# Kernel tuning notes

Measured on AMD Instinct MI355X. Metric: run time of the kernel, lower is better.

Reference implementation:

```python
import jax, jax.numpy as jnp
import numpy as np
from jax import lax

T = 1_000_000  # time steps
K = 64         # hidden states


def setup_inputs() -> dict:
    key = jax.random.key(0)
    k1, k2, k3, k4 = jax.random.split(key, 4)
    return {
        "y": jax.random.normal(k1, (T,), dtype=jnp.float32),
        "transition_logits": jax.random.normal(k2, (K, K), dtype=jnp.float32),
        "mu": jax.random.normal(k3, (K,), dtype=jnp.float32),
        "log_sigma": jax.random.normal(k4, (K,), dtype=jnp.float32) * 0.1,
    }


def _stationary_distribution(P):
    # Solve pi^T P = pi^T with sum(pi) = 1 via a linear system (differentiable).
    k = P.shape[0]
    A = jnp.transpose(P) - jnp.eye(k, dtype=P.dtype)
    A = A.at[-1, :].set(jnp.ones((k,), dtype=P.dtype))
    b = jnp.zeros((k,), dtype=P.dtype).at[-1].set(1.0)
    return jnp.linalg.solve(A, b)


def reference(y, transition_logits, mu, log_sigma):
    # Row-stochastic transition matrix [K, K]
    P = jax.nn.softmax(transition_logits, axis=-1)
    sigma = jnp.exp(log_sigma)  # [K]
    # Univariate Gaussian emission densities g[t, k] = N(y_t; mu_k, sigma_k^2)
    z = (y[:, None] - mu[None, :]) / sigma[None, :]           # [T, K]
    inv_norm = 1.0 / (sigma * jnp.sqrt(2.0 * jnp.pi))         # [K]
    g = jnp.exp(-0.5 * z * z) * inv_norm[None, :]             # [T, K]

    ut0 = _stationary_distribution(P)        # initial (predicted) distribution
    g0 = g[0]
    ft0 = jnp.sum(ut0 * g0)                  # normalizer at t=0
    utt0 = ut0 * g0 / ft0                    # filtered distribution at t=0

    def step(utt, gt):
        ut = utt @ P                         # predict: [K]
        num = ut * gt
        ft = jnp.sum(num)
        utt_new = num / ft                   # update (normalize)
        return utt_new, (ut, ft, utt_new)

    _, (Ut, ft_rest, Utt) = lax.scan(step, utt0, g[1:])

    ut = jnp.concatenate([ut0[None, :], Ut], axis=0)        # [T, K] predicted
    u_norm = jnp.concatenate([utt0[None, :], Utt], axis=0)  # [T, K] filtered
    ft = jnp.concatenate([ft0[None], ft_rest], axis=0)      # [T] normalizers
    return ut, u_norm, ft
```

## Files before the change

kernel.cpp:

```cpp
#include <hip/hip_runtime.h>

#define K 64
#define S_CHUNK 128
#define W_BURN 160
#define BATCH 16

typedef __attribute__((ext_vector_type(4))) _Float16 half4;
typedef __attribute__((ext_vector_type(4))) float f32x4;

__device__ __forceinline__ float waveReduceSum(float v) {
#pragma unroll
    for (int off = 32; off > 0; off >>= 1) v += __shfl_xor(v, off, 64);
    return v;
}

#define WS_P     0
#define WS_PI    4096
#define WS_UTT0  4160
#define WS_ISG   4224
#define WS_NNU   4288
#define WS_L2N   4352

__global__ __launch_bounds__(64) void hmm_setup(
    const float* __restrict__ y, const float* __restrict__ logits,
    const float* __restrict__ mu, const float* __restrict__ log_sigma,
    float* __restrict__ out, float* __restrict__ ws, int T)
{
    __shared__ float P[K][K];
    __shared__ float pib[K];
    const int k = threadIdx.x;

    float row[K]; float m = -3.4e38f;
#pragma unroll
    for (int i = 0; i < K; ++i) { row[i] = logits[k*K + i]; m = fmaxf(m, row[i]); }
    float s = 0.f;
#pragma unroll
    for (int i = 0; i < K; ++i) { row[i] = __expf(row[i] - m); s += row[i]; }
    float inv = 1.0f / s;
#pragma unroll
    for (int i = 0; i < K; ++i) { float p = row[i]*inv; P[k][i] = p; ws[WS_P + k*K + i] = p; }
    __syncthreads();

    pib[k] = 1.0f/64.0f;
    __syncthreads();
    for (int it = 0; it < 64; ++it) {
        float acc = 0.f;
#pragma unroll
        for (int j = 0; j < K; ++j) acc += pib[j]*P[j][k];
        float tot = waveReduceSum(acc);
        acc /= tot;
        __syncthreads();
        pib[k] = acc;
        __syncthreads();
    }
    float pi_k = pib[k];

    float mu_k = mu[k];
    float isg = __expf(-log_sigma[k]);
    float inorm = isg * 0.39894228040143267f;

    ws[WS_PI  + k] = pi_k;
    ws[WS_ISG + k] = isg;
    ws[WS_NNU + k] = -mu_k * isg;
    ws[WS_L2N + k] = __log2f(inorm);

    float y0 = y[0];
    float z = (y0 - mu_k) * isg;
    float g0 = __expf(-0.5f*z*z) * inorm;
    float num = pi_k * g0;
    float ft0 = waveReduceSum(num);
    float utt0 = num / ft0;
    ws[WS_UTT0 + k] = utt0;

    out[k] = pi_k;
    out[(size_t)T*K + k] = utt0;
    if (k == 0) out[(size_t)2*T*K] = ft0;
}

__global__ __launch_bounds__(64) void hmm_scan(
    const float* __restrict__ y, const float* __restrict__ ws,
    float* __restrict__ out, int T)
{
    const int lane = threadIdx.x;
    const int c = lane & 15;
    const int q = lane >> 4;
    const int NCH = (T + S_CHUNK - 1) / S_CHUNK;
    const int cg = blockIdx.x * BATCH + c;
    const int t0 = cg * S_CHUNK;

    half4 a[4][4];
#pragma unroll
    for (int nb = 0; nb < 4; ++nb)
#pragma unroll
        for (int kb = 0; kb < 4; ++kb)
#pragma unroll
            for (int j = 0; j < 4; ++j)
                a[nb][kb][j] = (_Float16)ws[WS_P + (16*kb + 4*q + j)*K + 16*nb + c];

    f32x4 isg_[4], nnu_[4], l2n_[4];
#pragma unroll
    for (int nb = 0; nb < 4; ++nb)
#pragma unroll
        for (int r = 0; r < 4; ++r) {
            int s = 16*nb + 4*q + r;
            isg_[nb][r] = ws[WS_ISG + s];
            nnu_[nb][r] = ws[WS_NNU + s];
            l2n_[nb][r] = ws[WS_L2N + s];
        }

    half4 bfr[4], u0h[4];
#pragma unroll
    for (int kb = 0; kb < 4; ++kb)
#pragma unroll
        for (int j = 0; j < 4; ++j) {
            int s = 16*kb + 4*q + j;
            bfr[kb][j] = (_Float16)ws[WS_PI + s];
            u0h[kb][j] = (_Float16)ws[WS_UTT0 + s];
        }

    const int tlo = (cg == 0) ? 1 : ((cg < NCH) ? 0 : 0x7fffffff);
    int tcur = t0 - W_BURN;

    float* po = out + (size_t)t0 * K + 4*q;
    float* pu = po + (size_t)T * K;
    float* pf = out + (size_t)2 * T * K + t0;

    int ib = min(max(tcur, 0), T - 4);
    f32x4 yv = *(const f32x4*)(y + ib);

#define STEP(OUTP, YCUR) do {                                                  \
    f32x4 acc[4] = {{0.f,0.f,0.f,0.f},{0.f,0.f,0.f,0.f},                       \
                    {0.f,0.f,0.f,0.f},{0.f,0.f,0.f,0.f}};                      \
    _Pragma("unroll")                                                          \
    for (int kb = 0; kb < 4; ++kb) {                                           \
        _Pragma("unroll")                                                      \
        for (int nb = 0; nb < 4; ++nb)                                         \
            acc[nb] = __builtin_amdgcn_mfma_f32_16x16x16f16(                   \
                a[nb][kb], bfr[kb], acc[nb], 0, 0, 0);                         \
    }                                                                          \
    const bool pred = (tcur >= tlo) & (tcur < T);                              \
    if (OUTP && pred) {                                                        \
        _Pragma("unroll")                                                      \
        for (int nb = 0; nb < 4; ++nb)                                         \
            *(f32x4*)(po + 16*nb) = acc[nb];                                   \
    }                                                                          \
    f32x4 nrm[4]; float st = 0.f;                                              \
    _Pragma("unroll")                                                          \
    for (int nb = 0; nb < 4; ++nb) {                                           \
        _Pragma("unroll")                                                      \
        for (int r = 0; r < 4; ++r) {                                          \
            float z  = fmaf(YCUR, isg_[nb][r], nnu_[nb][r]);                   \
            float ag = fmaf(z*z, -0.72134752f, l2n_[nb][r]);                   \
            float g  = __builtin_amdgcn_exp2f(ag);                             \
            nrm[nb][r] = acc[nb][r] * g;                                       \
            st += nrm[nb][r];                                                  \
        }                                                                      \
    }                                                                          \
    st += __shfl_xor(st, 16, 64);                                              \
    st += __shfl_xor(st, 32, 64);                                              \
    const float rs = __builtin_amdgcn_rcpf(st);                                \
    _Pragma("unroll")                                                          \
    for (int nb = 0; nb < 4; ++nb) nrm[nb] *= rs;                              \
    if (OUTP && pred) {                                                        \
        _Pragma("unroll")                                                      \
        for (int nb = 0; nb < 4; ++nb)                                         \
            *(f32x4*)(pu + 16*nb) = nrm[nb];                                   \
        if (lane < 16) *pf = st;                                               \
    }                                                                          \
    _Pragma("unroll")                                                          \
    for (int kb = 0; kb < 4; ++kb) {                                           \
        auto lo = __builtin_amdgcn_cvt_pkrtz(nrm[kb][0], nrm[kb][1]);          \
        auto hi = __builtin_amdgcn_cvt_pkrtz(nrm[kb][2], nrm[kb][3]);          \
        bfr[kb][0] = (_Float16)lo[0]; bfr[kb][1] = (_Float16)lo[1];            \
        bfr[kb][2] = (_Float16)hi[0]; bfr[kb][3] = (_Float16)hi[1];            \
    }                                                                          \
    if (OUTP) { po += K; pu += K; pf += 1; }                                   \
    ++tcur;                                                                    \
} while (0)

#pragma unroll 1
    for (int gi = 0; gi < W_BURN/4; ++gi) {
        int ibn = min(max(tcur + 4, 0), T - 4);
        f32x4 yn = *(const f32x4*)(y + ibn);
        STEP(0, yv[0]); STEP(0, yv[1]); STEP(0, yv[2]); STEP(0, yv[3]);
        yv = yn;
    }
    {
        int ibn = min(max(tcur + 4, 0), T - 4);
        f32x4 yn = *(const f32x4*)(y + ibn);
        STEP(1, yv[0]);
        if (cg == 0) { bfr[0]=u0h[0]; bfr[1]=u0h[1]; bfr[2]=u0h[2]; bfr[3]=u0h[3]; }
        STEP(1, yv[1]); STEP(1, yv[2]); STEP(1, yv[3]);
        yv = yn;
    }
#pragma unroll 1
    for (int gi = 1; gi < S_CHUNK/4; ++gi) {
        int ibn = min(max(tcur + 4, 0), T - 4);
        f32x4 yn = *(const f32x4*)(y + ibn);
        STEP(1, yv[0]); STEP(1, yv[1]); STEP(1, yv[2]); STEP(1, yv[3]);
        yv = yn;
    }
#undef STEP
}

extern "C" void kernel_launch(void* const* d_in, const int* in_sizes, int n_in,
                              void* d_out, int out_size, void* d_ws, size_t ws_size,
                              hipStream_t stream) {
    const float* y      = (const float*)d_in[0];
    const float* logits = (const float*)d_in[1];
    const float* mu     = (const float*)d_in[2];
    const float* lsig   = (const float*)d_in[3];
    float* out = (float*)d_out;
    float* ws  = (float*)d_ws;
    const int T = in_sizes[0];

    hmm_setup<<<1, 64, 0, stream>>>(y, logits, mu, lsig, out, ws, T);

    const int nch  = (T + S_CHUNK - 1) / S_CHUNK;
    const int nblk = (nch + BATCH - 1) / BATCH;
    hmm_scan<<<nblk, 64, 0, stream>>>(y, ws, out, T);
}
```

Before: 229.6 us.

## Defer normalization off the recurrence critical path with power-of-two rescaling

The step no longer normalizes the filtered vector before feeding it to the next matvec. The unnormalized product is fed straight back, and its scale is held in check by folding an exact power-of-two exponent into the emission exponent. The cross-lane sum, reciprocal and the outputs for the previous step are computed while the next step's MFMAs run. The MFMA chain is also split into two independent accumulators to shorten the dependency chain. This moves the shuffle-reduce and rcp latency off the serial chain. In exchange it adds extra bookkeeping, an epilogue store, and the risk of fp16 range or precision problems in the unnormalized values.

```diff
diff --git a/kernel.cpp b/kernel.cpp
--- a/kernel.cpp
+++ b/kernel.cpp
@@ -85,6 +85,7 @@
     const int c = lane & 15;
     const int q = lane >> 4;
     const int NCH = (T + S_CHUNK - 1) / S_CHUNK;
+    (void)NCH;
     const int cg = blockIdx.x * BATCH + c;
     const int t0 = cg * S_CHUNK;
 
@@ -118,63 +119,99 @@
             u0h[kb][j] = (_Float16)ws[WS_UTT0 + s];
         }
 
-    const int tlo = (cg == 0) ? 1 : ((cg < NCH) ? 0 : 0x7fffffff);
+    const int tlo = (cg == 0) ? 1 : 0;
     int tcur = t0 - W_BURN;
 
     float* po = out + (size_t)t0 * K + 4*q;
     float* pu = po + (size_t)T * K;
     float* pf = out + (size_t)2 * T * K + t0;
 
+    float h = 0.25f;
+    float rmP = 1.0f;
+    f32x4 nbP[4] = {{0.f,0.f,0.f,0.f},{0.f,0.f,0.f,0.f},
+                    {0.f,0.f,0.f,0.f},{0.f,0.f,0.f,0.f}};
+
     int ib = min(max(tcur, 0), T - 4);
     f32x4 yv = *(const f32x4*)(y + ib);
 
-#define STEP(OUTP, YCUR) do {                                                  \
-    f32x4 acc[4] = {{0.f,0.f,0.f,0.f},{0.f,0.f,0.f,0.f},                       \
-                    {0.f,0.f,0.f,0.f},{0.f,0.f,0.f,0.f}};                      \
-    _Pragma("unroll")                                                          \
-    for (int kb = 0; kb < 4; ++kb) {                                           \
+#define STEP(OUTC, OUTPV, YCUR) do {                                           \
+                                  \
+    f32x4 accA_[4] = {{0.f,0.f,0.f,0.f},{0.f,0.f,0.f,0.f},                     \
+                      {0.f,0.f,0.f,0.f},{0.f,0.f,0.f,0.f}};                    \
+    f32x4 accB_[4] = {{0.f,0.f,0.f,0.f},{0.f,0.f,0.f,0.f},                     \
+                      {0.f,0.f,0.f,0.f},{0.f,0.f,0.f,0.f}};                    \
+    _Pragma("unroll")                                                          \
+    for (int nb_ = 0; nb_ < 4; ++nb_)                                          \
+        accA_[nb_] = __builtin_amdgcn_mfma_f32_16x16x16f16(a[nb_][0], bfr[0], accA_[nb_], 0,0,0); \
+    _Pragma("unroll")                                                          \
+    for (int nb_ = 0; nb_ < 4; ++nb_)                                          \
+        accB_[nb_] = __builtin_amdgcn_mfma_f32_16x16x16f16(a[nb_][2], bfr[2], accB_[nb_], 0,0,0); \
+    _Pragma("unroll")                                                          \
+    for (int nb_ = 0; nb_ < 4; ++nb_)                                          \
+        accA_[nb_] = __builtin_amdgcn_mfma_f32_16x16x16f16(a[nb_][1], bfr[1], accA_[nb_], 0,0,0); \
+    _Pragma("unroll")                                                          \
+    for (int nb_ = 0; nb_ < 4; ++nb_)                                          \
+        accB_[nb_] = __builtin_amdgcn_mfma_f32_16x16x16f16(a[nb_][3], bfr[3], accB_[nb_], 0,0,0); \
+                         \
+    float s1_ = h + __shfl_xor(h, 16, 64);                                     \
+    float stP_ = s1_ + __shfl_xor(s1_, 32, 64);                                \
+    float rsP_ = __builtin_amdgcn_rcpf(stP_);                                  \
+    float ftprev_ = stP_ * rmP;                                                \
+    unsigned ub_ = __float_as_uint(stP_);                                      \
+    float xf_ = (float)(127 - (int)((ub_ >> 23) & 255u));                      \
+    float mant_ = __uint_as_float((ub_ & 0x007fffffu) | 0x3f800000u);          \
+    float rmN_ = __builtin_amdgcn_rcpf(mant_);                                 \
+                \
+    f32x4 g_[4];                                                               \
+    _Pragma("unroll")                                                          \
+    for (int nb_ = 0; nb_ < 4; ++nb_) {                                        \
+        f32x4 z_ = YCUR * isg_[nb_] + nnu_[nb_];                               \
+        f32x4 ag_ = z_*z_*(-0.72134752f) + l2n_[nb_] + xf_;                    \
         _Pragma("unroll")                                                      \
-        for (int nb = 0; nb < 4; ++nb)                                         \
-            acc[nb] = __builtin_amdgcn_mfma_f32_16x16x16f16(                   \
-                a[nb][kb], bfr[kb], acc[nb], 0, 0, 0);                         \
-    }                                                                          \
-    const bool pred = (tcur >= tlo) & (tcur < T);                              \
-    if (OUTP && pred) {                                                        \
-        _Pragma("unroll")                                                      \
-        for (int nb = 0; nb < 4; ++nb)                                         \
-            *(f32x4*)(po + 16*nb) = acc[nb];                                   \
-    }                                                                          \
-    f32x4 nrm[4]; float st = 0.f;                                              \
-    _Pragma("unroll")                                                          \
-    for (int nb = 0; nb < 4; ++nb) {                                           \
-        _Pragma("unroll")                                                      \
-        for (int r = 0; r < 4; ++r) {                                          \
-            float z  = fmaf(YCUR, isg_[nb][r], nnu_[nb][r]);                   \
-            float ag = fmaf(z*z, -0.72134752f, l2n_[nb][r]);                   \
-            float g  = __builtin_amdgcn_exp2f(ag);                             \
-            nrm[nb][r] = acc[nb][r] * g;                                       \
-            st += nrm[nb][r];                                                  \
+        for (int r_ = 0; r_ < 4; ++r_) g_[nb_][r_] = __builtin_amdgcn_exp2f(ag_[r_]); \
+    }                                                                          \
+                                  \
+    if (OUTPV) {                                                               \
+        const bool pp_ = ((tcur-1) >= tlo) & ((tcur-1) < T);                   \
+        if (pp_) {                                                             \
+            _Pragma("unroll")                                                  \
+            for (int nb_ = 0; nb_ < 4; ++nb_)                                  \
+                *(f32x4*)(pu - K + 16*nb_) = nbP[nb_] * rsP_;                  \
+            if (lane < 16) pf[-1] = ftprev_;                                   \
         }                                                                      \
     }                                                                          \
-    st += __shfl_xor(st, 16, 64);                                              \
-    st += __shfl_xor(st, 32, 64);                                              \
-    const float rs = __builtin_amdgcn_rcpf(st);                                \
-    _Pragma("unroll")                                                          \
-    for (int nb = 0; nb < 4; ++nb) nrm[nb] *= rs;                              \
-    if (OUTP && pred) {                                                        \
-        _Pragma("unroll")                                                      \
-        for (int nb = 0; nb < 4; ++nb)                                         \
-            *(f32x4*)(pu + 16*nb) = nrm[nb];                                   \
-        if (lane < 16) *pf = st;                                               \
-    }                                                                          \
-    _Pragma("unroll")                                                          \
-    for (int kb = 0; kb < 4; ++kb) {                                           \
-        auto lo = __builtin_amdgcn_cvt_pkrtz(nrm[kb][0], nrm[kb][1]);          \
-        auto hi = __builtin_amdgcn_cvt_pkrtz(nrm[kb][2], nrm[kb][3]);          \
-        bfr[kb][0] = (_Float16)lo[0]; bfr[kb][1] = (_Float16)lo[1];            \
-        bfr[kb][2] = (_Float16)hi[0]; bfr[kb][3] = (_Float16)hi[1];            \
-    }                                                                          \
-    if (OUTP) { po += K; pu += K; pf += 1; }                                   \
+                                               \
+    f32x4 acc_[4], nbv_[4];                                                    \
+    _Pragma("unroll")                                                          \
+    for (int nb_ = 0; nb_ < 4; ++nb_) acc_[nb_] = accA_[nb_] + accB_[nb_];     \
+    _Pragma("unroll")                                                          \
+    for (int nb_ = 0; nb_ < 4; ++nb_) nbv_[nb_] = acc_[nb_] * g_[nb_];         \
+    _Pragma("unroll")                                                          \
+    for (int kb_ = 0; kb_ < 4; ++kb_) {                                        \
+        auto lo_ = __builtin_amdgcn_cvt_pkrtz(nbv_[kb_][0], nbv_[kb_][1]);     \
+        auto hi_ = __builtin_amdgcn_cvt_pkrtz(nbv_[kb_][2], nbv_[kb_][3]);     \
+        bfr[kb_][0] = (_Float16)lo_[0]; bfr[kb_][1] = (_Float16)lo_[1];        \
+        bfr[kb_][2] = (_Float16)hi_[0]; bfr[kb_][3] = (_Float16)hi_[1];        \
+    }                                                                          \
+                                          \
+    if (OUTC) {                                                                \
+        const bool pc_ = (tcur >= tlo) & (tcur < T);                           \
+        if (pc_) {                                                             \
+            _Pragma("unroll")                                                  \
+            for (int nb_ = 0; nb_ < 4; ++nb_)                                  \
+                *(f32x4*)(po + 16*nb_) = acc_[nb_] * rsP_;                     \
+        }                                                                      \
+    }                                                                          \
+               \
+    {                                                                          \
+        f32x4 sA_ = nbv_[0] + nbv_[1];                                         \
+        f32x4 sB_ = nbv_[2] + nbv_[3];                                         \
+        f32x4 sC_ = sA_ + sB_;                                                 \
+        h = (sC_[0] + sC_[1]) + (sC_[2] + sC_[3]);                             \
+    }                                                                          \
+    nbP[0]=nbv_[0]; nbP[1]=nbv_[1]; nbP[2]=nbv_[2]; nbP[3]=nbv_[3];            \
+    rmP = rmN_;                                                                \
+    if (OUTC) { po += K; pu += K; pf += 1; }                                   \
     ++tcur;                                                                    \
 } while (0)
 
@@ -182,25 +219,42 @@
     for (int gi = 0; gi < W_BURN/4; ++gi) {
         int ibn = min(max(tcur + 4, 0), T - 4);
         f32x4 yn = *(const f32x4*)(y + ibn);
-        STEP(0, yv[0]); STEP(0, yv[1]); STEP(0, yv[2]); STEP(0, yv[3]);
+        STEP(0,0, yv[0]); STEP(0,0, yv[1]); STEP(0,0, yv[2]); STEP(0,0, yv[3]);
         yv = yn;
     }
     {
         int ibn = min(max(tcur + 4, 0), T - 4);
         f32x4 yn = *(const f32x4*)(y + ibn);
-        STEP(1, yv[0]);
-        if (cg == 0) { bfr[0]=u0h[0]; bfr[1]=u0h[1]; bfr[2]=u0h[2]; bfr[3]=u0h[3]; }
-        STEP(1, yv[1]); STEP(1, yv[2]); STEP(1, yv[3]);
+        STEP(1,0, yv[0]);
+        if (cg == 0) {
+            bfr[0]=u0h[0]; bfr[1]=u0h[1]; bfr[2]=u0h[2]; bfr[3]=u0h[3];
+            h = 0.25f;
+        }
+        STEP(1,1, yv[1]); STEP(1,1, yv[2]); STEP(1,1, yv[3]);
         yv = yn;
     }
 #pragma unroll 1
     for (int gi = 1; gi < S_CHUNK/4; ++gi) {
         int ibn = min(max(tcur + 4, 0), T - 4);
         f32x4 yn = *(const f32x4*)(y + ibn);
-        STEP(1, yv[0]); STEP(1, yv[1]); STEP(1, yv[2]); STEP(1, yv[3]);
+        STEP(1,1, yv[0]); STEP(1,1, yv[1]); STEP(1,1, yv[2]); STEP(1,1, yv[3]);
         yv = yn;
     }
 #undef STEP
+
+    {
+        float s1 = h + __shfl_xor(h, 16, 64);
+        float stL = s1 + __shfl_xor(s1, 32, 64);
+        float rsL = __builtin_amdgcn_rcpf(stL);
+        float ftL = stL * rmP;
+        const bool pp = ((tcur-1) >= tlo) & ((tcur-1) < T);
+        if (pp) {
+#pragma unroll
+            for (int nb = 0; nb < 4; ++nb)
+                *(f32x4*)(pu - K + 16*nb) = nbP[nb] * rsL;
+            if (lane < 16) pf[-1] = ftL;
+        }
+    }
 }
 
 extern "C" void kernel_launch(void* const* d_in, const int* in_sizes, int n_in,
```

Result: no change. 231.2 us (+0.7%).

## Replace MFMA batched scan with per-wave fdot2 matvec via LDS broadcast

Applied to the files above, without the earlier changes.

Restructures the chunked HMM filter so each half-wave owns one chunk and each lane computes two states using packed fp16 dot products against register-resident P columns. The state vector is shared through LDS instead of being fed to MFMA. Normalization is deferred: each step folds an exponent-based rescale into the emission term and emits the previous step's filtered output using the next step's sum. Burn-in drops from 160 to 128 steps and blocks grow to 256 threads, trading MFMA throughput for far more independent chunks in flight and less per-step reduction latency. The extra fp16 sums and deferred scaling add some precision risk.

```diff
diff --git a/kernel.cpp b/kernel.cpp
--- a/kernel.cpp
+++ b/kernel.cpp
@@ -2,16 +2,35 @@
 
 #define K 64
 #define S_CHUNK 128
-#define W_BURN 160
-#define BATCH 16
-
-typedef __attribute__((ext_vector_type(4))) _Float16 half4;
+#define W_BURN 128
+
+typedef __attribute__((ext_vector_type(2))) _Float16 half2v;
+typedef __attribute__((ext_vector_type(8))) _Float16 half8;
 typedef __attribute__((ext_vector_type(4))) float f32x4;
+typedef __attribute__((ext_vector_type(2))) float f32x2;
+typedef __attribute__((ext_vector_type(4))) unsigned u32x4;
+
+#define ONEPK 0x3C003C00u
 
 __device__ __forceinline__ float waveReduceSum(float v) {
 #pragma unroll
     for (int off = 32; off > 0; off >>= 1) v += __shfl_xor(v, off, 64);
     return v;
+}
+
+__device__ __forceinline__ unsigned pkh(float a, float b) {
+    auto t = __builtin_amdgcn_cvt_pkrtz(a, b);
+    return __builtin_bit_cast(unsigned, t);
+}
+
+__device__ __forceinline__ float fdot2(unsigned a, unsigned b, float c) {
+#if __has_builtin(__builtin_amdgcn_fdot2)
+    return __builtin_amdgcn_fdot2(__builtin_bit_cast(half2v, a),
+                                  __builtin_bit_cast(half2v, b), c, false);
+#else
+    half2v x = __builtin_bit_cast(half2v, a), y = __builtin_bit_cast(half2v, b);
+    return c + (float)x[0] * (float)y[0] + (float)x[1] * (float)y[1];
+#endif
 }
 
 #define WS_P     0
@@ -20,6 +39,7 @@
 #define WS_ISG   4224
 #define WS_NNU   4288
 #define WS_L2N   4352
+#define WS_PKP   4480
 
 __global__ __launch_bounds__(64) void hmm_setup(
     const float* __restrict__ y, const float* __restrict__ logits,
@@ -55,6 +75,11 @@
     }
     float pi_k = pib[k];
 
+    unsigned* wsu = (unsigned*)ws;
+#pragma unroll
+    for (int j2 = 0; j2 < 32; ++j2)
+        wsu[WS_PKP + k*32 + j2] = pkh(P[2*j2][k], P[2*j2+1][k]);
+
     float mu_k = mu[k];
     float isg = __expf(-log_sigma[k]);
     float inorm = isg * 0.39894228040143267f;
@@ -77,130 +102,137 @@
     if (k == 0) out[(size_t)2*T*K] = ft0;
 }
 
-__global__ __launch_bounds__(64) void hmm_scan(
+__global__ __launch_bounds__(256, 2) void hmm_scan(
     const float* __restrict__ y, const float* __restrict__ ws,
     float* __restrict__ out, int T)
 {
-    const int lane = threadIdx.x;
-    const int c = lane & 15;
-    const int q = lane >> 4;
-    const int NCH = (T + S_CHUNK - 1) / S_CHUNK;
-    const int cg = blockIdx.x * BATCH + c;
-    const int t0 = cg * S_CHUNK;
-
-    half4 a[4][4];
-#pragma unroll
-    for (int nb = 0; nb < 4; ++nb)
-#pragma unroll
-        for (int kb = 0; kb < 4; ++kb)
-#pragma unroll
-            for (int j = 0; j < 4; ++j)
-                a[nb][kb][j] = (_Float16)ws[WS_P + (16*kb + 4*q + j)*K + 16*nb + c];
-
-    f32x4 isg_[4], nnu_[4], l2n_[4];
-#pragma unroll
-    for (int nb = 0; nb < 4; ++nb)
-#pragma unroll
-        for (int r = 0; r < 4; ++r) {
-            int s = 16*nb + 4*q + r;
-            isg_[nb][r] = ws[WS_ISG + s];
-            nnu_[nb][r] = ws[WS_NNU + s];
-            l2n_[nb][r] = ws[WS_L2N + s];
+    __shared__ __align__(16) unsigned ubuf[4][2][32];
+    const int tid  = threadIdx.x;
+    const int wid  = tid >> 6;
+    const int lane = tid & 63;
+    const int h    = lane >> 5;
+    const int r    = lane & 31;
+    const int s0   = 2 * r;
+    const int wv   = blockIdx.x * 4 + wid;
+    const int cg   = 2 * wv + h;
+    const int t0   = cg * S_CHUNK;
+
+    const unsigned* wsu = (const unsigned*)ws;
+
+    u32x4 P0r[8], P1r[8];
+    {
+        const u32x4* p0 = (const u32x4*)(wsu + WS_PKP + s0 * 32);
+        const u32x4* p1 = (const u32x4*)(wsu + WS_PKP + (s0 + 1) * 32);
+#pragma unroll
+        for (int i = 0; i < 8; ++i) { P0r[i] = p0[i]; P1r[i] = p1[i]; }
+    }
+
+    const float isg0 = ws[WS_ISG + s0], isg1 = ws[WS_ISG + s0 + 1];
+    const float nnu0 = ws[WS_NNU + s0], nnu1 = ws[WS_NNU + s0 + 1];
+    const float l2n0 = ws[WS_L2N + s0], l2n1 = ws[WS_L2N + s0 + 1];
+
+    unsigned* ub = &ubuf[wid][h][0];
+    const u32x4* ubv = (const u32x4*)ub;
+
+    unsigned myu = pkh(ws[WS_PI + s0], ws[WS_PI + s0 + 1]);
+    ub[r] = myu;
+    unsigned u0pk = pkh(ws[WS_UTT0 + s0], ws[WS_UTT0 + s0 + 1]);
+
+    const int tlo = (cg == 0) ? 1 : t0;
+    const bool is_cg0 = (cg == 0);
+    const int t_end = t0 + S_CHUNK;
+
+    float* po = out + (size_t)(t0 - W_BURN) * K + s0;
+    float* pu = po + (size_t)T * K;
+    float* pf = out + (size_t)2 * T * K + (t0 - W_BURN);
+
+    float rcpPrev = 1.0f, sclPrev = 1.0f;
+
+#pragma unroll 1
+    for (int t = t0 - W_BURN; t < t_end; ++t) {
+        int iy = min(max(t, 0), T - 1);
+        float yc = y[iy];
+
+        u32x4 bj[8];
+#pragma unroll
+        for (int i = 0; i < 8; ++i) bj[i] = ubv[i];
+
+        half8 h0 = __builtin_bit_cast(half8, bj[0]) + __builtin_bit_cast(half8, bj[1]);
+        half8 h1 = __builtin_bit_cast(half8, bj[2]) + __builtin_bit_cast(half8, bj[3]);
+        half8 h2 = __builtin_bit_cast(half8, bj[4]) + __builtin_bit_cast(half8, bj[5]);
+        half8 h3 = __builtin_bit_cast(half8, bj[6]) + __builtin_bit_cast(half8, bj[7]);
+        h0 = h0 + h2; h1 = h1 + h3;
+        u32x4 w0 = __builtin_bit_cast(u32x4, h0), w1 = __builtin_bit_cast(u32x4, h1);
+        float su = 0.f;
+        su = fdot2(w0[0], ONEPK, su); su = fdot2(w0[1], ONEPK, su);
+        su = fdot2(w0[2], ONEPK, su); su = fdot2(w0[3], ONEPK, su);
+        su = fdot2(w1[0], ONEPK, su); su = fdot2(w1[1], ONEPK, su);
+        su = fdot2(w1[2], ONEPK, su); su = fdot2(w1[3], ONEPK, su);
+
+        float a0 = 0.f, a1 = 0.f, b0 = 0.f, b1 = 0.f;
+#pragma unroll
+        for (int i = 0; i < 8; ++i) {
+            u32x4 w = bj[i];
+            a0 = fdot2(w[0], P0r[i][0], a0);  b0 = fdot2(w[0], P1r[i][0], b0);
+            a1 = fdot2(w[1], P0r[i][1], a1);  b1 = fdot2(w[1], P1r[i][1], b1);
+            a0 = fdot2(w[2], P0r[i][2], a0);  b0 = fdot2(w[2], P1r[i][2], b0);
+            a1 = fdot2(w[3], P0r[i][3], a1);  b1 = fdot2(w[3], P1r[i][3], b1);
         }
-
-    half4 bfr[4], u0h[4];
-#pragma unroll
-    for (int kb = 0; kb < 4; ++kb)
-#pragma unroll
-        for (int j = 0; j < 4; ++j) {
-            int s = 16*kb + 4*q + j;
-            bfr[kb][j] = (_Float16)ws[WS_PI + s];
-            u0h[kb][j] = (_Float16)ws[WS_UTT0 + s];
+        float v0 = a0 + a1, v1 = b0 + b1;
+
+        unsigned sb = __float_as_uint(su);
+        int eb = (int)((sb >> 23) & 255u);
+        float xf = (float)(126 - eb);
+        float scl = __uint_as_float((unsigned)(eb + 1) << 23);
+        float rs = __builtin_amdgcn_rcpf(su);
+
+        float z0 = fmaf(yc, isg0, nnu0);
+        float z1 = fmaf(yc, isg1, nnu1);
+        float g0 = __builtin_amdgcn_exp2f(fmaf(z0 * z0, -0.72134752f, l2n0 + xf));
+        float g1 = __builtin_amdgcn_exp2f(fmaf(z1 * z1, -0.72134752f, l2n1 + xf));
+        float nb0 = v0 * g0, nb1 = v1 * g1;
+
+        const bool outc = (t >= tlo) & (t < T);
+        const bool outp = ((t - 1) >= tlo) & ((t - 1) < T);
+        if (outc) *(f32x2*)po = f32x2{v0 * rs, v1 * rs};
+        if (outp) {
+            half2v mu2 = __builtin_bit_cast(half2v, myu);
+            *(f32x2*)(pu - K) = f32x2{(float)mu2[0] * rs, (float)mu2[1] * rs};
+            if (r == 0) pf[-1] = su * rcpPrev * sclPrev;
         }
 
-    const int tlo = (cg == 0) ? 1 : ((cg < NCH) ? 0 : 0x7fffffff);
-    int tcur = t0 - W_BURN;
-
-    float* po = out + (size_t)t0 * K + 4*q;
-    float* pu = po + (size_t)T * K;
-    float* pf = out + (size_t)2 * T * K + t0;
-
-    int ib = min(max(tcur, 0), T - 4);
-    f32x4 yv = *(const f32x4*)(y + ib);
-
-#define STEP(OUTP, YCUR) do {                                                  \
-    f32x4 acc[4] = {{0.f,0.f,0.f,0.f},{0.f,0.f,0.f,0.f},                       \
-                    {0.f,0.f,0.f,0.f},{0.f,0.f,0.f,0.f}};                      \
-    _Pragma("unroll")                                                          \
-    for (int kb = 0; kb < 4; ++kb) {                                           \
-        _Pragma("unroll")                                                      \
-        for (int nb = 0; nb < 4; ++nb)                                         \
-            acc[nb] = __builtin_amdgcn_mfma_f32_16x16x16f16(                   \
-                a[nb][kb], bfr[kb], acc[nb], 0, 0, 0);                         \
-    }                                                                          \
-    const bool pred = (tcur >= tlo) & (tcur < T);                              \
-    if (OUTP && pred) {                                                        \
-        _Pragma("unroll")                                                      \
-        for (int nb = 0; nb < 4; ++nb)                                         \
-            *(f32x4*)(po + 16*nb) = acc[nb];                                   \
-    }                                                                          \
-    f32x4 nrm[4]; float st = 0.f;                                              \
-    _Pragma("unroll")                                                          \
-    for (int nb = 0; nb < 4; ++nb) {                                           \
-        _Pragma("unroll")                                                      \
-        for (int r = 0; r < 4; ++r) {                                          \
-            float z  = fmaf(YCUR, isg_[nb][r], nnu_[nb][r]);                   \
-            float ag = fmaf(z*z, -0.72134752f, l2n_[nb][r]);                   \
-            float g  = __builtin_amdgcn_exp2f(ag);                             \
-            nrm[nb][r] = acc[nb][r] * g;                                       \
-            st += nrm[nb][r];                                                  \
-        }                                                                      \
-    }                                                                          \
-    st += __shfl_xor(st, 16, 64);                                              \
-    st += __shfl_xor(st, 32, 64);                                              \
-    const float rs = __builtin_amdgcn_rcpf(st);                                \
-    _Pragma("unroll")                                                          \
-    for (int nb = 0; nb < 4; ++nb) nrm[nb] *= rs;                              \
-    if (OUTP && pred) {                                                        \
-        _Pragma("unroll")                                                      \
-        for (int nb = 0; nb < 4; ++nb)                                         \
-            *(f32x4*)(pu + 16*nb) = nrm[nb];                                   \
-        if (lane < 16) *pf = st;                                               \
-    }                                                                          \
-    _Pragma("unroll")                                                          \
-    for (int kb = 0; kb < 4; ++kb) {                                           \
-        auto lo = __builtin_amdgcn_cvt_pkrtz(nrm[kb][0], nrm[kb][1]);          \
-        auto hi = __builtin_amdgcn_cvt_pkrtz(nrm[kb][2], nrm[kb][3]);          \
-        bfr[kb][0] = (_Float16)lo[0]; bfr[kb][1] = (_Float16)lo[1];            \
-        bfr[kb][2] = (_Float16)hi[0]; bfr[kb][3] = (_Float16)hi[1];            \
-    }                                                                          \
-    if (OUTP) { po += K; pu += K; pf += 1; }                                   \
-    ++tcur;                                                                    \
-} while (0)
-
-#pragma unroll 1
-    for (int gi = 0; gi < W_BURN/4; ++gi) {
-        int ibn = min(max(tcur + 4, 0), T - 4);
-        f32x4 yn = *(const f32x4*)(y + ibn);
-        STEP(0, yv[0]); STEP(0, yv[1]); STEP(0, yv[2]); STEP(0, yv[3]);
-        yv = yn;
-    }
+        myu = pkh(nb0, nb1);
+        ub[r] = myu;
+        rcpPrev = rs; sclPrev = scl;
+
+        if (is_cg0 & (t == 0)) { myu = u0pk; ub[r] = myu; }
+
+        po += K; pu += K; pf += 1;
+    }
+
     {
-        int ibn = min(max(tcur + 4, 0), T - 4);
-        f32x4 yn = *(const f32x4*)(y + ibn);
-        STEP(1, yv[0]);
-        if (cg == 0) { bfr[0]=u0h[0]; bfr[1]=u0h[1]; bfr[2]=u0h[2]; bfr[3]=u0h[3]; }
-        STEP(1, yv[1]); STEP(1, yv[2]); STEP(1, yv[3]);
-        yv = yn;
-    }
-#pragma unroll 1
-    for (int gi = 1; gi < S_CHUNK/4; ++gi) {
-        int ibn = min(max(tcur + 4, 0), T - 4);
-        f32x4 yn = *(const f32x4*)(y + ibn);
-        STEP(1, yv[0]); STEP(1, yv[1]); STEP(1, yv[2]); STEP(1, yv[3]);
-        yv = yn;
-    }
-#undef STEP
+        u32x4 bj[8];
+#pragma unroll
+        for (int i = 0; i < 8; ++i) bj[i] = ubv[i];
+        half8 h0 = __builtin_bit_cast(half8, bj[0]) + __builtin_bit_cast(half8, bj[1]);
+        half8 h1 = __builtin_bit_cast(half8, bj[2]) + __builtin_bit_cast(half8, bj[3]);
+        half8 h2 = __builtin_bit_cast(half8, bj[4]) + __builtin_bit_cast(half8, bj[5]);
+        half8 h3 = __builtin_bit_cast(half8, bj[6]) + __builtin_bit_cast(half8, bj[7]);
+        h0 = h0 + h2; h1 = h1 + h3;
+        u32x4 w0 = __builtin_bit_cast(u32x4, h0), w1 = __builtin_bit_cast(u32x4, h1);
+        float su = 0.f;
+        su = fdot2(w0[0], ONEPK, su); su = fdot2(w0[1], ONEPK, su);
+        su = fdot2(w0[2], ONEPK, su); su = fdot2(w0[3], ONEPK, su);
+        su = fdot2(w1[0], ONEPK, su); su = fdot2(w1[1], ONEPK, su);
+        su = fdot2(w1[2], ONEPK, su); su = fdot2(w1[3], ONEPK, su);
+        float rs = __builtin_amdgcn_rcpf(su);
+        const bool outp = ((t_end - 1) >= tlo) & ((t_end - 1) < T);
+        if (outp) {
+            half2v mu2 = __builtin_bit_cast(half2v, myu);
+            *(f32x2*)(pu - K) = f32x2{(float)mu2[0] * rs, (float)mu2[1] * rs};
+            if (r == 0) pf[-1] = su * rcpPrev * sclPrev;
+        }
+    }
 }
 
 extern "C" void kernel_launch(void* const* d_in, const int* in_sizes, int n_in,
@@ -216,7 +248,8 @@
 
     hmm_setup<<<1, 64, 0, stream>>>(y, logits, mu, lsig, out, ws, T);
 
-    const int nch  = (T + S_CHUNK - 1) / S_CHUNK;
-    const int nblk = (nch + BATCH - 1) / BATCH;
-    hmm_scan<<<nblk, 64, 0, stream>>>(y, ws, out, T);
-}
+    const int nch    = (T + S_CHUNK - 1) / S_CHUNK;
+    const int nwaves = (nch + 1) / 2;
+    const int nblk   = (nwaves + 3) / 4;
+    hmm_scan<<<nblk, 256, 0, stream>>>(y, ws, out, T);
+}
```

After: 359.1 us. 56.4% more time.
